# Optimization experiments

Hardware: AMD Instinct MI355X
Metric: run time of the kernel (lower is better)

Reference implementation:

```python
import jax, jax.numpy as jnp
import numpy as np

N = 50000      # nodes
E = 400000     # edges (before self-loops)
NFEAT = 256
NHID = 64
NHEAD = 8
NOUT = 128


def gat_conv(h, src, dst, W, attn_l, attn_r, bias, n, H, D):
    """DGL GATConv (eval mode: feat_drop/attn_drop are no-ops), negative_slope=0.2."""
    feat = (h @ W).reshape(n, H, D)                      # [N,H,D]
    el = jnp.einsum('nhd,hd->nh', feat, attn_l)          # [N,H]
    er = jnp.einsum('nhd,hd->nh', feat, attn_r)          # [N,H]
    e = jax.nn.leaky_relu(el[src] + er[dst], 0.2)        # [E,H]
    # segment softmax over incoming edges of each dst node
    m = jax.ops.segment_max(e, dst, num_segments=n)      # [N,H] (every node has a self-loop)
    ex = jnp.exp(e - m[dst])
    denom = jax.ops.segment_sum(ex, dst, num_segments=n)
    a = ex / denom[dst]                                  # [E,H]
    rst = jax.ops.segment_sum(a[:, :, None] * feat[src], dst, num_segments=n)  # [N,H,D]
    return rst + bias.reshape(1, H, D)


def setup_inputs() -> dict:
    key = jax.random.key(0)
    ks = jax.random.split(key, 10)
    s = 0.1
    x = jax.random.normal(ks[0], (N, NFEAT), jnp.float32)
    edge_index = jax.random.randint(ks[1], (2, E), 0, N, dtype=jnp.int64)
    W1 = jax.random.normal(ks[2], (NFEAT, NHEAD * NHID), jnp.float32) * s
    al1 = jax.random.normal(ks[3], (NHEAD, NHID), jnp.float32) * s
    ar1 = jax.random.normal(ks[4], (NHEAD, NHID), jnp.float32) * s
    b1 = jax.random.normal(ks[5], (NHEAD * NHID,), jnp.float32) * s
    W2 = jax.random.normal(ks[6], (NHEAD * NHID, NOUT), jnp.float32) * s
    al2 = jax.random.normal(ks[7], (1, NOUT), jnp.float32) * s
    ar2 = jax.random.normal(ks[8], (1, NOUT), jnp.float32) * s
    b2 = jax.random.normal(ks[9], (NOUT,), jnp.float32) * s
    return {"x": x, "edge_index": edge_index, "W1": W1, "al1": al1, "ar1": ar1,
            "b1": b1, "W2": W2, "al2": al2, "ar2": ar2, "b2": b2}


def reference(x, edge_index, W1, al1, ar1, b1, W2, al2, ar2, b2):
    n = x.shape[0]
    loop = jnp.arange(n, dtype=edge_index.dtype)
    src = jnp.concatenate([edge_index[0], loop])  # dgl.add_self_loop
    dst = jnp.concatenate([edge_index[1], loop])
    # hidden layer (dropout is identity in eval mode)
    h = gat_conv(x, src, dst, W1, al1, ar1, b1, n, NHEAD, NHID).reshape(n, NFEAT * 2)
    h = jax.nn.elu(h)
    out = gat_conv(h, src, dst, W2, al2, ar2, b2, n, 1, NOUT).reshape(n, NOUT)
    return out
```

## Files before the change

kernel.cpp:

```cpp
#include <hip/hip_runtime.h>

#define NFEAT 256
#define NHID 64
#define NHEAD 8
#define HID1 512
#define NOUT 128

typedef unsigned short ushort_t;
typedef unsigned int uint_t;
typedef __attribute__((ext_vector_type(8))) short short8;
typedef __attribute__((ext_vector_type(4))) float floatx4;
typedef __attribute__((ext_vector_type(4))) ushort_t ushort4_t;

static __device__ __forceinline__ float bf2f(uint_t s) {
    return __uint_as_float(s << 16);
}
static __device__ __forceinline__ ushort_t f2bf(float f) {
    uint_t u = __float_as_uint(f);
    u += 0x7FFF + ((u >> 16) & 1);
    return (ushort_t)(u >> 16);
}

__global__ void k_hist(const int* __restrict__ dstA, int E, int n, int* __restrict__ deg) {
    int i = blockIdx.x * blockDim.x + threadIdx.x;
    if (i >= E + n) return;
    int d = (i < E) ? dstA[i] : (i - E);
    atomicAdd(&deg[d], 1);
}

__global__ __launch_bounds__(1024) void k_scan(const int* __restrict__ deg, int* __restrict__ indptr, int n) {
    __shared__ int part[1024];
    int t = threadIdx.x;
    int chunk = (n + 1023) >> 10;
    int b = t * chunk;
    int e = min(b + chunk, n);
    int s = 0;
    for (int i = b; i < e; ++i) s += deg[i];
    part[t] = s;
    __syncthreads();
    for (int off = 1; off < 1024; off <<= 1) {
        int v = (t >= off) ? part[t - off] : 0;
        __syncthreads();
        part[t] += v;
        __syncthreads();
    }
    int run = (t == 0) ? 0 : part[t - 1];
    for (int i = b; i < e; ++i) { indptr[i] = run; run += deg[i]; }
    if (t == 1023) indptr[n] = part[1023];
}

__global__ void k_fill(const int* __restrict__ srcA, const int* __restrict__ dstA, int E, int n,
                       const int* __restrict__ indptr, int* __restrict__ cnt,
                       int* __restrict__ csr_src, int* __restrict__ csr_dst) {
    int i = blockIdx.x * blockDim.x + threadIdx.x;
    if (i >= E + n) return;
    int s, d;
    if (i < E) { s = srcA[i]; d = dstA[i]; } else { s = i - E; d = s; }
    int pos = indptr[d] + atomicAdd(&cnt[d], 1);
    csr_src[pos] = s;
    csr_dst[pos] = d;
}

__global__ void k_cast(const float* __restrict__ x, ushort_t* __restrict__ xb, int total4) {
    int i = blockIdx.x * blockDim.x + threadIdx.x;
    if (i >= total4) return;
    floatx4 f = ((const floatx4*)x)[i];
    ushort4_t o;
    #pragma unroll
    for (int j = 0; j < 4; ++j) o[j] = f2bf(f[j]);
    ((ushort4_t*)xb)[i] = o;
}

__global__ void k_prepw(const float* __restrict__ W, ushort_t* __restrict__ Wt, int K, int N) {
    int i = blockIdx.x * blockDim.x + threadIdx.x;
    if (i >= K * N) return;
    int nn = i / K, kk = i % K;
    Wt[i] = f2bf(W[(size_t)kk * N + nn]);
}

__global__ __launch_bounds__(256) void k_gemm128(const ushort_t* __restrict__ A,
                                                 const ushort_t* __restrict__ Bt,
                                                 ushort_t* __restrict__ C,
                                                 int M, int N, int K) {
    __shared__ __align__(16) ushort_t As[128 * 32];
    __shared__ __align__(16) ushort_t Bs[128 * 32];
    const int t = threadIdx.x;
    const int w = t >> 6, lane = t & 63;
    const int l16 = lane & 15, quad = lane >> 4;
    const int m0 = blockIdx.y * 128, n0 = blockIdx.x * 128;
    const int r0 = (w >> 1) * 64;
    const int c0 = (w & 1) * 64;

    floatx4 acc[4][4] = {};

    const int srow[2] = { (0 * 256 + t) >> 2, (1 * 256 + t) >> 2 };
    const int skp = (t & 3) * 8;
    const int wbase0 = (0 * 256 + (t & ~63)) * 8;
    const int wbase1 = (1 * 256 + (t & ~63)) * 8;

    for (int k0 = 0; k0 < K; k0 += 32) {
        {
            int gr0 = m0 + srow[0]; if (gr0 >= M) gr0 = M - 1;
            int gr1 = m0 + srow[1]; if (gr1 >= M) gr1 = M - 1;
            const ushort_t* gpa0 = A + (size_t)gr0 * K + k0 + skp;
            const ushort_t* gpa1 = A + (size_t)gr1 * K + k0 + skp;
            const ushort_t* gpb0 = Bt + (size_t)(n0 + srow[0]) * K + k0 + skp;
            const ushort_t* gpb1 = Bt + (size_t)(n0 + srow[1]) * K + k0 + skp;
            __builtin_amdgcn_global_load_lds((const __attribute__((address_space(1))) void*)gpa0,
                (__attribute__((address_space(3))) void*)(As + wbase0), 16, 0, 0);
            __builtin_amdgcn_global_load_lds((const __attribute__((address_space(1))) void*)gpa1,
                (__attribute__((address_space(3))) void*)(As + wbase1), 16, 0, 0);
            __builtin_amdgcn_global_load_lds((const __attribute__((address_space(1))) void*)gpb0,
                (__attribute__((address_space(3))) void*)(Bs + wbase0), 16, 0, 0);
            __builtin_amdgcn_global_load_lds((const __attribute__((address_space(1))) void*)gpb1,
                (__attribute__((address_space(3))) void*)(Bs + wbase1), 16, 0, 0);
        }
        __syncthreads();

        short8 af[4], bf[4];
        #pragma unroll
        for (int i = 0; i < 4; ++i)
            af[i] = *(const short8*)(As + (r0 + i * 16 + l16) * 32 + quad * 8);
        #pragma unroll
        for (int j = 0; j < 4; ++j)
            bf[j] = *(const short8*)(Bs + (c0 + j * 16 + l16) * 32 + quad * 8);
        #pragma unroll
        for (int i = 0; i < 4; ++i)
            #pragma unroll
            for (int j = 0; j < 4; ++j)
                acc[i][j] = __builtin_amdgcn_mfma_f32_16x16x32_bf16(af[i], bf[j], acc[i][j], 0, 0, 0);
        __syncthreads();
    }

    #pragma unroll
    for (int i = 0; i < 4; ++i) {
        #pragma unroll
        for (int r = 0; r < 4; ++r) {
            int row = m0 + r0 + i * 16 + quad * 4 + r;
            if (row < M) {
                #pragma unroll
                for (int j = 0; j < 4; ++j)
                    C[(size_t)row * N + n0 + c0 + j * 16 + l16] = f2bf(acc[i][j][r]);
            }
        }
    }
}

__global__ __launch_bounds__(256) void k_elr1(const uint_t* __restrict__ fb, const float* __restrict__ al,
                                              const float* __restrict__ ar, float* __restrict__ el,
                                              float* __restrict__ er, int n) {
    int node = blockIdx.x;
    int t = threadIdx.x;
    uint_t u = fb[(size_t)node * 256 + t];
    float lo = bf2f(u & 0xFFFF), hi = bf2f(u >> 16);
    float p = lo * al[2 * t] + hi * al[2 * t + 1];
    float q = lo * ar[2 * t] + hi * ar[2 * t + 1];
    for (int o = 16; o > 0; o >>= 1) {
        p += __shfl_down(p, o, 32);
        q += __shfl_down(q, o, 32);
    }
    if ((t & 31) == 0) {
        int h = t >> 5;
        el[node * NHEAD + h] = p;
        er[node * NHEAD + h] = q;
    }
}

__global__ void k_wgt1(const int* __restrict__ csr_src, const int* __restrict__ csr_dst,
                       const float* __restrict__ el, const float* __restrict__ er,
                       float* __restrict__ wcsr, int ET) {
    int idx = blockIdx.x * blockDim.x + threadIdx.x;
    if (idx >= ET * NHEAD) return;
    int e = idx >> 3, h = idx & 7;
    int s = csr_src[e], d = csr_dst[e];
    float x = el[s * NHEAD + h] + er[d * NHEAD + h];
    x = (x > 0.f) ? x : 0.2f * x;
    wcsr[idx] = __expf(x);
}

__global__ void k_wgt2(const int* __restrict__ csr_src, const int* __restrict__ csr_dst,
                       const float* __restrict__ el2, const float* __restrict__ er2,
                       float* __restrict__ wcsr, int ET) {
    int e = blockIdx.x * blockDim.x + threadIdx.x;
    if (e >= ET) return;
    int s = csr_src[e], d = csr_dst[e];
    float x = el2[s] + er2[d];
    x = (x > 0.f) ? x : 0.2f * x;
    wcsr[e] = __expf(x);
}

__global__ __launch_bounds__(256) void k_agg1(const uint_t* __restrict__ fb, const float* __restrict__ wcsr,
                                              const float* __restrict__ b1,
                                              const int* __restrict__ indptr, const int* __restrict__ csr_src,
                                              uint_t* __restrict__ h1b, int n) {
    int node = blockIdx.x;
    int t = threadIdx.x;
    int h = t >> 5;
    int e0 = indptr[node], e1 = indptr[node + 1];
    float a0 = 0.f, a1 = 0.f, den = 0.f;
    int e = e0;
    for (; e + 3 < e1; e += 4) {
        int s0 = csr_src[e], s1 = csr_src[e + 1], s2 = csr_src[e + 2], s3 = csr_src[e + 3];
        float w0 = wcsr[(size_t)e * NHEAD + h];
        float w1 = wcsr[(size_t)(e + 1) * NHEAD + h];
        float w2 = wcsr[(size_t)(e + 2) * NHEAD + h];
        float w3 = wcsr[(size_t)(e + 3) * NHEAD + h];
        uint_t u0 = fb[(size_t)s0 * 256 + t];
        uint_t u1 = fb[(size_t)s1 * 256 + t];
        uint_t u2 = fb[(size_t)s2 * 256 + t];
        uint_t u3 = fb[(size_t)s3 * 256 + t];
        den += (w0 + w1) + (w2 + w3);
        a0 += w0 * bf2f(u0 & 0xFFFF) + w1 * bf2f(u1 & 0xFFFF)
            + w2 * bf2f(u2 & 0xFFFF) + w3 * bf2f(u3 & 0xFFFF);
        a1 += w0 * bf2f(u0 >> 16) + w1 * bf2f(u1 >> 16)
            + w2 * bf2f(u2 >> 16) + w3 * bf2f(u3 >> 16);
    }
    for (; e < e1; ++e) {
        int s = csr_src[e];
        float w = wcsr[(size_t)e * NHEAD + h];
        uint_t u = fb[(size_t)s * 256 + t];
        den += w;
        a0 += w * bf2f(u & 0xFFFF);
        a1 += w * bf2f(u >> 16);
    }
    float inv = 1.f / den;
    float v0 = a0 * inv + b1[2 * t];
    float v1 = a1 * inv + b1[2 * t + 1];
    v0 = (v0 > 0.f) ? v0 : (__expf(v0) - 1.f);
    v1 = (v1 > 0.f) ? v1 : (__expf(v1) - 1.f);
    h1b[(size_t)node * 256 + t] = (uint_t)f2bf(v0) | ((uint_t)f2bf(v1) << 16);
}

__global__ __launch_bounds__(256) void k_elr2(const uint_t* __restrict__ fb2, const float* __restrict__ al2,
                                              const float* __restrict__ ar2, float* __restrict__ el2,
                                              float* __restrict__ er2, int n) {
    int wid = blockIdx.x * 4 + (threadIdx.x >> 6);
    int lane = threadIdx.x & 63;
    if (wid >= n) return;
    uint_t u = fb2[(size_t)wid * 64 + lane];
    float lo = bf2f(u & 0xFFFF), hi = bf2f(u >> 16);
    float p = lo * al2[2 * lane] + hi * al2[2 * lane + 1];
    float q = lo * ar2[2 * lane] + hi * ar2[2 * lane + 1];
    for (int o = 32; o > 0; o >>= 1) { p += __shfl_down(p, o); q += __shfl_down(q, o); }
    if (lane == 0) { el2[wid] = p; er2[wid] = q; }
}

__global__ __launch_bounds__(256) void k_agg2(const uint_t* __restrict__ fb2, const float* __restrict__ wcsr,
                                              const float* __restrict__ b2,
                                              const int* __restrict__ indptr, const int* __restrict__ csr_src,
                                              float* __restrict__ out, int n) {
    int wid = blockIdx.x * 4 + (threadIdx.x >> 6);
    int lane = threadIdx.x & 63;
    if (wid >= n) return;
    int e0 = indptr[wid], e1 = indptr[wid + 1];
    float a0 = 0.f, a1 = 0.f, den = 0.f;
    int e = e0;
    for (; e + 3 < e1; e += 4) {
        int s0 = csr_src[e], s1 = csr_src[e + 1], s2 = csr_src[e + 2], s3 = csr_src[e + 3];
        float w0 = wcsr[e], w1 = wcsr[e + 1], w2 = wcsr[e + 2], w3 = wcsr[e + 3];
        uint_t u0 = fb2[(size_t)s0 * 64 + lane];
        uint_t u1 = fb2[(size_t)s1 * 64 + lane];
        uint_t u2 = fb2[(size_t)s2 * 64 + lane];
        uint_t u3 = fb2[(size_t)s3 * 64 + lane];
        den += (w0 + w1) + (w2 + w3);
        a0 += w0 * bf2f(u0 & 0xFFFF) + w1 * bf2f(u1 & 0xFFFF)
            + w2 * bf2f(u2 & 0xFFFF) + w3 * bf2f(u3 & 0xFFFF);
        a1 += w0 * bf2f(u0 >> 16) + w1 * bf2f(u1 >> 16)
            + w2 * bf2f(u2 >> 16) + w3 * bf2f(u3 >> 16);
    }
    for (; e < e1; ++e) {
        int s = csr_src[e];
        float w = wcsr[e];
        uint_t u = fb2[(size_t)s * 64 + lane];
        den += w;
        a0 += w * bf2f(u & 0xFFFF);
        a1 += w * bf2f(u >> 16);
    }
    float inv = 1.f / den;
    float2 o;
    o.x = a0 * inv + b2[2 * lane];
    o.y = a1 * inv + b2[2 * lane + 1];
    ((float2*)out)[(size_t)wid * 64 + lane] = o;
}

extern "C" void kernel_launch(void* const* d_in, const int* in_sizes, int n_in,
                              void* d_out, int out_size, void* d_ws, size_t ws_size,
                              hipStream_t stream) {
    const float* x   = (const float*)d_in[0];
    const int*   ei  = (const int*)d_in[1];
    const float* W1  = (const float*)d_in[2];
    const float* al1 = (const float*)d_in[3];
    const float* ar1 = (const float*)d_in[4];
    const float* b1  = (const float*)d_in[5];
    const float* W2  = (const float*)d_in[6];
    const float* al2 = (const float*)d_in[7];
    const float* ar2 = (const float*)d_in[8];
    const float* b2  = (const float*)d_in[9];

    const int n  = in_sizes[0] / NFEAT;
    const int E  = in_sizes[1] / 2;
    const int ET = E + n;
    const int* srcA = ei;
    const int* dstA = ei + E;

    char* ws = (char*)d_ws;
    size_t off = 0;
    auto alloc = [&](size_t bytes) -> void* {
        void* p = ws + off;
        off += (bytes + 255) & ~(size_t)255;
        return p;
    };
    ushort_t* xb     = (ushort_t*)alloc((size_t)n * NFEAT * 2);
    ushort_t* feat1b = (ushort_t*)alloc((size_t)n * HID1 * 2);
    ushort_t* h1b    = (ushort_t*)alloc((size_t)n * HID1 * 2);
    ushort_t* feat2b = (ushort_t*)alloc((size_t)n * NOUT * 2);
    ushort_t* W1t    = (ushort_t*)alloc((size_t)NFEAT * HID1 * 2);
    ushort_t* W2t    = (ushort_t*)alloc((size_t)HID1 * NOUT * 2);
    float* el1 = (float*)alloc((size_t)n * NHEAD * 4);
    float* er1 = (float*)alloc((size_t)n * NHEAD * 4);
    float* el2 = (float*)alloc((size_t)n * 4);
    float* er2 = (float*)alloc((size_t)n * 4);
    float* wcsr1 = (float*)alloc((size_t)ET * NHEAD * 4);
    float* wcsr2 = (float*)alloc((size_t)ET * 4);
    int* indptr  = (int*)alloc((size_t)(n + 1) * 4);
    int* deg     = (int*)alloc((size_t)n * 4);
    int* cnt     = (int*)alloc((size_t)n * 4);
    int* csr     = (int*)alloc((size_t)ET * 4);
    int* csrd    = (int*)alloc((size_t)ET * 4);

    hipMemsetAsync(deg, 0, (size_t)n * 4, stream);
    hipMemsetAsync(cnt, 0, (size_t)n * 4, stream);

    k_hist<<<(ET + 255) / 256, 256, 0, stream>>>(dstA, E, n, deg);
    k_scan<<<1, 1024, 0, stream>>>(deg, indptr, n);
    k_fill<<<(ET + 255) / 256, 256, 0, stream>>>(srcA, dstA, E, n, indptr, cnt, csr, csrd);

    k_cast<<<((n * NFEAT / 4) + 255) / 256, 256, 0, stream>>>(x, xb, n * NFEAT / 4);
    k_prepw<<<(NFEAT * HID1 + 255) / 256, 256, 0, stream>>>(W1, W1t, NFEAT, HID1);
    k_prepw<<<(HID1 * NOUT + 255) / 256, 256, 0, stream>>>(W2, W2t, HID1, NOUT);

    k_gemm128<<<dim3(HID1 / 128, (n + 127) / 128), 256, 0, stream>>>(xb, W1t, feat1b, n, HID1, NFEAT);
    k_elr1<<<n, 256, 0, stream>>>((const uint_t*)feat1b, al1, ar1, el1, er1, n);
    k_wgt1<<<(ET * NHEAD + 255) / 256, 256, 0, stream>>>(csr, csrd, el1, er1, wcsr1, ET);
    k_agg1<<<n, 256, 0, stream>>>((const uint_t*)feat1b, wcsr1, b1, indptr, csr, (uint_t*)h1b, n);

    k_gemm128<<<dim3(NOUT / 128, (n + 127) / 128), 256, 0, stream>>>(h1b, W2t, feat2b, n, NOUT, HID1);
    k_elr2<<<(n + 3) / 4, 256, 0, stream>>>((const uint_t*)feat2b, al2, ar2, el2, er2, n);
    k_wgt2<<<(ET + 255) / 256, 256, 0, stream>>>(csr, csrd, el2, er2, wcsr2, ET);
    k_agg2<<<(n + 3) / 4, 256, 0, stream>>>((const uint_t*)feat2b, wcsr2, b2, indptr, csr, (float*)d_out, n);
}
```

Measured before the change: 442.6 us.

## Fuse attention-logit dot products into GEMM epilogues and merge prep kernels

Computes el/er per node and head directly from the fp32 GEMM accumulators in both projection GEMMs, using intra-16-lane shuffles, which removes the separate k_elr1/k_elr2 passes that reread the bf16 features. The second GEMM gets a 64-row tile to launch more blocks for the narrow 128-column output. The input cast, both weight transposes and the degree histogram are merged into one launch. The scan loops are unrolled by four. Logits now come from fp32 accumulators instead of bf16-rounded features, which changes numerics slightly.

```diff
diff --git a/kernel.cpp b/kernel.cpp
--- a/kernel.cpp
+++ b/kernel.cpp
@@ -21,11 +21,35 @@
     return (ushort_t)(u >> 16);
 }
 
-__global__ void k_hist(const int* __restrict__ dstA, int E, int n, int* __restrict__ deg) {
-    int i = blockIdx.x * blockDim.x + threadIdx.x;
-    if (i >= E + n) return;
-    int d = (i < E) ? dstA[i] : (i - E);
-    atomicAdd(&deg[d], 1);
+__global__ void k_prep(const float* __restrict__ x, ushort_t* __restrict__ xb,
+                       const float* __restrict__ W1, ushort_t* __restrict__ W1t,
+                       const float* __restrict__ W2, ushort_t* __restrict__ W2t,
+                       const int* __restrict__ dstA, int* __restrict__ deg,
+                       int n, int E, int c0, int c1, int c2) {
+    int blk = blockIdx.x;
+    int t = threadIdx.x;
+    if (blk < c0) {
+        int i = blk * 256 + t;
+        floatx4 f = ((const floatx4*)x)[i];
+        ushort4_t o;
+        #pragma unroll
+        for (int j = 0; j < 4; ++j) o[j] = f2bf(f[j]);
+        ((ushort4_t*)xb)[i] = o;
+    } else if (blk < c1) {
+        int i = (blk - c0) * 256 + t;
+        int nn = i / NFEAT, kk = i % NFEAT;
+        W1t[i] = f2bf(W1[(size_t)kk * HID1 + nn]);
+    } else if (blk < c2) {
+        int i = (blk - c1) * 256 + t;
+        int nn = i / HID1, kk = i % HID1;
+        W2t[i] = f2bf(W2[(size_t)kk * NOUT + nn]);
+    } else {
+        int i = (blk - c2) * 256 + t;
+        if (i < E + n) {
+            int d = (i < E) ? dstA[i] : (i - E);
+            atomicAdd(&deg[d], 1);
+        }
+    }
 }
 
 __global__ __launch_bounds__(1024) void k_scan(const int* __restrict__ deg, int* __restrict__ indptr, int n) {
@@ -35,7 +59,10 @@
     int b = t * chunk;
     int e = min(b + chunk, n);
     int s = 0;
-    for (int i = b; i < e; ++i) s += deg[i];
+    int i = b;
+    for (; i + 3 < e; i += 4)
+        s += (deg[i] + deg[i + 1]) + (deg[i + 2] + deg[i + 3]);
+    for (; i < e; ++i) s += deg[i];
     part[t] = s;
     __syncthreads();
     for (int off = 1; off < 1024; off <<= 1) {
@@ -45,7 +72,15 @@
         __syncthreads();
     }
     int run = (t == 0) ? 0 : part[t - 1];
-    for (int i = b; i < e; ++i) { indptr[i] = run; run += deg[i]; }
+    i = b;
+    for (; i + 3 < e; i += 4) {
+        int d0 = deg[i], d1 = deg[i + 1], d2 = deg[i + 2], d3 = deg[i + 3];
+        indptr[i] = run; run += d0;
+        indptr[i + 1] = run; run += d1;
+        indptr[i + 2] = run; run += d2;
+        indptr[i + 3] = run; run += d3;
+    }
+    for (; i < e; ++i) { indptr[i] = run; run += deg[i]; }
     if (t == 1023) indptr[n] = part[1023];
 }
 
@@ -61,27 +96,14 @@
     csr_dst[pos] = d;
 }
 
-__global__ void k_cast(const float* __restrict__ x, ushort_t* __restrict__ xb, int total4) {
-    int i = blockIdx.x * blockDim.x + threadIdx.x;
-    if (i >= total4) return;
-    floatx4 f = ((const floatx4*)x)[i];
-    ushort4_t o;
-    #pragma unroll
-    for (int j = 0; j < 4; ++j) o[j] = f2bf(f[j]);
-    ((ushort4_t*)xb)[i] = o;
-}
-
-__global__ void k_prepw(const float* __restrict__ W, ushort_t* __restrict__ Wt, int K, int N) {
-    int i = blockIdx.x * blockDim.x + threadIdx.x;
-    if (i >= K * N) return;
-    int nn = i / K, kk = i % K;
-    Wt[i] = f2bf(W[(size_t)kk * N + nn]);
-}
-
-__global__ __launch_bounds__(256) void k_gemm128(const ushort_t* __restrict__ A,
-                                                 const ushort_t* __restrict__ Bt,
-                                                 ushort_t* __restrict__ C,
-                                                 int M, int N, int K) {
+__global__ __launch_bounds__(256) void k_gemm1(const ushort_t* __restrict__ A,
+                                               const ushort_t* __restrict__ Bt,
+                                               ushort_t* __restrict__ C,
+                                               const float* __restrict__ al,
+                                               const float* __restrict__ ar,
+                                               float* __restrict__ el, float* __restrict__ er,
+                                               int M) {
+    const int N = HID1, K = NFEAT;
     __shared__ __align__(16) ushort_t As[128 * 32];
     __shared__ __align__(16) ushort_t Bs[128 * 32];
     const int t = threadIdx.x;
@@ -99,22 +121,20 @@
     const int wbase1 = (1 * 256 + (t & ~63)) * 8;
 
     for (int k0 = 0; k0 < K; k0 += 32) {
-        {
-            int gr0 = m0 + srow[0]; if (gr0 >= M) gr0 = M - 1;
-            int gr1 = m0 + srow[1]; if (gr1 >= M) gr1 = M - 1;
-            const ushort_t* gpa0 = A + (size_t)gr0 * K + k0 + skp;
-            const ushort_t* gpa1 = A + (size_t)gr1 * K + k0 + skp;
-            const ushort_t* gpb0 = Bt + (size_t)(n0 + srow[0]) * K + k0 + skp;
-            const ushort_t* gpb1 = Bt + (size_t)(n0 + srow[1]) * K + k0 + skp;
-            __builtin_amdgcn_global_load_lds((const __attribute__((address_space(1))) void*)gpa0,
-                (__attribute__((address_space(3))) void*)(As + wbase0), 16, 0, 0);
-            __builtin_amdgcn_global_load_lds((const __attribute__((address_space(1))) void*)gpa1,
-                (__attribute__((address_space(3))) void*)(As + wbase1), 16, 0, 0);
-            __builtin_amdgcn_global_load_lds((const __attribute__((address_space(1))) void*)gpb0,
-                (__attribute__((address_space(3))) void*)(Bs + wbase0), 16, 0, 0);
-            __builtin_amdgcn_global_load_lds((const __attribute__((address_space(1))) void*)gpb1,
-                (__attribute__((address_space(3))) void*)(Bs + wbase1), 16, 0, 0);
-        }
+        int gr0 = m0 + srow[0]; if (gr0 >= M) gr0 = M - 1;
+        int gr1 = m0 + srow[1]; if (gr1 >= M) gr1 = M - 1;
+        const ushort_t* gpa0 = A + (size_t)gr0 * K + k0 + skp;
+        const ushort_t* gpa1 = A + (size_t)gr1 * K + k0 + skp;
+        const ushort_t* gpb0 = Bt + (size_t)(n0 + srow[0]) * K + k0 + skp;
+        const ushort_t* gpb1 = Bt + (size_t)(n0 + srow[1]) * K + k0 + skp;
+        __builtin_amdgcn_global_load_lds((const __attribute__((address_space(1))) void*)gpa0,
+            (__attribute__((address_space(3))) void*)(As + wbase0), 16, 0, 0);
+        __builtin_amdgcn_global_load_lds((const __attribute__((address_space(1))) void*)gpa1,
+            (__attribute__((address_space(3))) void*)(As + wbase1), 16, 0, 0);
+        __builtin_amdgcn_global_load_lds((const __attribute__((address_space(1))) void*)gpb0,
+            (__attribute__((address_space(3))) void*)(Bs + wbase0), 16, 0, 0);
+        __builtin_amdgcn_global_load_lds((const __attribute__((address_space(1))) void*)gpb1,
+            (__attribute__((address_space(3))) void*)(Bs + wbase1), 16, 0, 0);
         __syncthreads();
 
         short8 af[4], bf[4];
@@ -144,25 +164,134 @@
             }
         }
     }
-}
-
-__global__ __launch_bounds__(256) void k_elr1(const uint_t* __restrict__ fb, const float* __restrict__ al,
-                                              const float* __restrict__ ar, float* __restrict__ el,
-                                              float* __restrict__ er, int n) {
-    int node = blockIdx.x;
-    int t = threadIdx.x;
-    uint_t u = fb[(size_t)node * 256 + t];
-    float lo = bf2f(u & 0xFFFF), hi = bf2f(u >> 16);
-    float p = lo * al[2 * t] + hi * al[2 * t + 1];
-    float q = lo * ar[2 * t] + hi * ar[2 * t + 1];
-    for (int o = 16; o > 0; o >>= 1) {
-        p += __shfl_down(p, o, 32);
-        q += __shfl_down(q, o, 32);
-    }
-    if ((t & 31) == 0) {
-        int h = t >> 5;
-        el[node * NHEAD + h] = p;
-        er[node * NHEAD + h] = q;
+
+    float alv[4], arv[4];
+    #pragma unroll
+    for (int j = 0; j < 4; ++j) {
+        int col = n0 + c0 + j * 16 + l16;
+        alv[j] = al[col];
+        arv[j] = ar[col];
+    }
+    int head = (n0 + c0) >> 6;
+    #pragma unroll
+    for (int i = 0; i < 4; ++i) {
+        #pragma unroll
+        for (int r = 0; r < 4; ++r) {
+            float p = acc[i][0][r] * alv[0] + acc[i][1][r] * alv[1]
+                    + acc[i][2][r] * alv[2] + acc[i][3][r] * alv[3];
+            float q = acc[i][0][r] * arv[0] + acc[i][1][r] * arv[1]
+                    + acc[i][2][r] * arv[2] + acc[i][3][r] * arv[3];
+            #pragma unroll
+            for (int o = 8; o > 0; o >>= 1) {
+                p += __shfl_down(p, o);
+                q += __shfl_down(q, o);
+            }
+            if (l16 == 0) {
+                int row = m0 + r0 + i * 16 + quad * 4 + r;
+                if (row < M) {
+                    el[row * NHEAD + head] = p;
+                    er[row * NHEAD + head] = q;
+                }
+            }
+        }
+    }
+}
+
+__global__ __launch_bounds__(256) void k_gemm2(const ushort_t* __restrict__ A,
+                                               const ushort_t* __restrict__ Bt,
+                                               ushort_t* __restrict__ C,
+                                               const float* __restrict__ al,
+                                               const float* __restrict__ ar,
+                                               float* __restrict__ el, float* __restrict__ er,
+                                               int M) {
+    const int N = NOUT, K = HID1;
+    __shared__ __align__(16) ushort_t As[64 * 32];
+    __shared__ __align__(16) ushort_t Bs[128 * 32];
+    __shared__ float elp[64][2], erp[64][2];
+    const int t = threadIdx.x;
+    const int w = t >> 6, lane = t & 63;
+    const int l16 = lane & 15, quad = lane >> 4;
+    const int m0 = blockIdx.y * 64;
+    const int r0 = (w >> 1) * 32;
+    const int c0 = (w & 1) * 64;
+
+    floatx4 acc[2][4] = {};
+
+    const int arow = t >> 2;
+    const int brow[2] = { (0 * 256 + t) >> 2, (1 * 256 + t) >> 2 };
+    const int skp = (t & 3) * 8;
+    const int wbaseA = (t & ~63) * 8;
+    const int wbase0 = (0 * 256 + (t & ~63)) * 8;
+    const int wbase1 = (1 * 256 + (t & ~63)) * 8;
+
+    for (int k0 = 0; k0 < K; k0 += 32) {
+        int gr = m0 + arow; if (gr >= M) gr = M - 1;
+        const ushort_t* gpa = A + (size_t)gr * K + k0 + skp;
+        const ushort_t* gpb0 = Bt + (size_t)brow[0] * K + k0 + skp;
+        const ushort_t* gpb1 = Bt + (size_t)brow[1] * K + k0 + skp;
+        __builtin_amdgcn_global_load_lds((const __attribute__((address_space(1))) void*)gpa,
+            (__attribute__((address_space(3))) void*)(As + wbaseA), 16, 0, 0);
+        __builtin_amdgcn_global_load_lds((const __attribute__((address_space(1))) void*)gpb0,
+            (__attribute__((address_space(3))) void*)(Bs + wbase0), 16, 0, 0);
+        __builtin_amdgcn_global_load_lds((const __attribute__((address_space(1))) void*)gpb1,
+            (__attribute__((address_space(3))) void*)(Bs + wbase1), 16, 0, 0);
+        __syncthreads();
+
+        short8 af[2], bf[4];
+        #pragma unroll
+        for (int i = 0; i < 2; ++i)
+            af[i] = *(const short8*)(As + (r0 + i * 16 + l16) * 32 + quad * 8);
+        #pragma unroll
+        for (int j = 0; j < 4; ++j)
+            bf[j] = *(const short8*)(Bs + (c0 + j * 16 + l16) * 32 + quad * 8);
+        #pragma unroll
+        for (int i = 0; i < 2; ++i)
+            #pragma unroll
+            for (int j = 0; j < 4; ++j)
+                acc[i][j] = __builtin_amdgcn_mfma_f32_16x16x32_bf16(af[i], bf[j], acc[i][j], 0, 0, 0);
+        __syncthreads();
+    }
+
+    float alv[4], arv[4];
+    #pragma unroll
+    for (int j = 0; j < 4; ++j) {
+        int col = c0 + j * 16 + l16;
+        alv[j] = al[col];
+        arv[j] = ar[col];
+    }
+    #pragma unroll
+    for (int i = 0; i < 2; ++i) {
+        #pragma unroll
+        for (int r = 0; r < 4; ++r) {
+            int lrow = r0 + i * 16 + quad * 4 + r;
+            int row = m0 + lrow;
+            if (row < M) {
+                #pragma unroll
+                for (int j = 0; j < 4; ++j)
+                    C[(size_t)row * N + c0 + j * 16 + l16] = f2bf(acc[i][j][r]);
+            }
+            float p = acc[i][0][r] * alv[0] + acc[i][1][r] * alv[1]
+                    + acc[i][2][r] * alv[2] + acc[i][3][r] * alv[3];
+            float q = acc[i][0][r] * arv[0] + acc[i][1][r] * arv[1]
+                    + acc[i][2][r] * arv[2] + acc[i][3][r] * arv[3];
+            #pragma unroll
+            for (int o = 8; o > 0; o >>= 1) {
+                p += __shfl_down(p, o);
+                q += __shfl_down(q, o);
+            }
+            if (l16 == 0) {
+                elp[lrow][w & 1] = p;
+                erp[lrow][w & 1] = q;
+            }
+        }
+    }
+    __syncthreads();
+    if (t < 64) {
+        int row = m0 + t;
+        if (row < M) {
+            el[row] = elp[t][0] + elp[t][1];
+            er[row] = erp[t][0] + erp[t][1];
+        }
     }
 }
 
@@ -231,20 +360,6 @@
     h1b[(size_t)node * 256 + t] = (uint_t)f2bf(v0) | ((uint_t)f2bf(v1) << 16);
 }
 
-__global__ __launch_bounds__(256) void k_elr2(const uint_t* __restrict__ fb2, const float* __restrict__ al2,
-                                              const float* __restrict__ ar2, float* __restrict__ el2,
-                                              float* __restrict__ er2, int n) {
-    int wid = blockIdx.x * 4 + (threadIdx.x >> 6);
-    int lane = threadIdx.x & 63;
-    if (wid >= n) return;
-    uint_t u = fb2[(size_t)wid * 64 + lane];
-    float lo = bf2f(u & 0xFFFF), hi = bf2f(u >> 16);
-    float p = lo * al2[2 * lane] + hi * al2[2 * lane + 1];
-    float q = lo * ar2[2 * lane] + hi * ar2[2 * lane + 1];
-    for (int o = 32; o > 0; o >>= 1) { p += __shfl_down(p, o); q += __shfl_down(q, o); }
-    if (lane == 0) { el2[wid] = p; er2[wid] = q; }
-}
-
 __global__ __launch_bounds__(256) void k_agg2(const uint_t* __restrict__ fb2, const float* __restrict__ wcsr,
                                               const float* __restrict__ b2,
                                               const int* __restrict__ indptr, const int* __restrict__ csr_src,
@@ -331,21 +446,20 @@
     hipMemsetAsync(deg, 0, (size_t)n * 4, stream);
     hipMemsetAsync(cnt, 0, (size_t)n * 4, stream);
 
-    k_hist<<<(ET + 255) / 256, 256, 0, stream>>>(dstA, E, n, deg);
+    const int c0 = (n * NFEAT / 4) / 256;
+    const int c1 = c0 + (NFEAT * HID1) / 256;
+    const int c2 = c1 + (HID1 * NOUT) / 256;
+    const int c3 = c2 + (ET + 255) / 256;
+    k_prep<<<c3, 256, 0, stream>>>(x, xb, W1, W1t, W2, W2t, dstA, deg, n, E, c0, c1, c2);
+
     k_scan<<<1, 1024, 0, stream>>>(deg, indptr, n);
     k_fill<<<(ET + 255) / 256, 256, 0, stream>>>(srcA, dstA, E, n, indptr, cnt, csr, csrd);
 
-    k_cast<<<((n * NFEAT / 4) + 255) / 256, 256, 0, stream>>>(x, xb, n * NFEAT / 4);
-    k_prepw<<<(NFEAT * HID1 + 255) / 256, 256, 0, stream>>>(W1, W1t, NFEAT, HID1);
-    k_prepw<<<(HID1 * NOUT + 255) / 256, 256, 0, stream>>>(W2, W2t, HID1, NOUT);
-
-    k_gemm128<<<dim3(HID1 / 128, (n + 127) / 128), 256, 0, stream>>>(xb, W1t, feat1b, n, HID1, NFEAT);
-    k_elr1<<<n, 256, 0, stream>>>((const uint_t*)feat1b, al1, ar1, el1, er1, n);
+    k_gemm1<<<dim3(HID1 / 128, (n + 127) / 128), 256, 0, stream>>>(xb, W1t, feat1b, al1, ar1, el1, er1, n);
     k_wgt1<<<(ET * NHEAD + 255) / 256, 256, 0, stream>>>(csr, csrd, el1, er1, wcsr1, ET);
     k_agg1<<<n, 256, 0, stream>>>((const uint_t*)feat1b, wcsr1, b1, indptr, csr, (uint_t*)h1b, n);
 
-    k_gemm128<<<dim3(NOUT / 128, (n + 127) / 128), 256, 0, stream>>>(h1b, W2t, feat2b, n, NOUT, HID1);
-    k_elr2<<<(n + 3) / 4, 256, 0, stream>>>((const uint_t*)feat2b, al2, ar2, el2, er2, n);
+    k_gemm2<<<dim3(1, (n + 63) / 64), 256, 0, stream>>>(h1b, W2t, feat2b, al2, ar2, el2, er2, n);
     k_wgt2<<<(ET + 255) / 256, 256, 0, stream>>>(csr, csrd, el2, er2, wcsr2, ET);
     k_agg2<<<(n + 3) / 4, 256, 0, stream>>>((const uint_t*)feat2b, wcsr2, b2, indptr, csr, (float*)d_out, n);
 }
```

New measurement: 386.7 us. 1.14x faster.
